# Kernel tuning notes

Measured on AMD Instinct MI355X. Metric: run time of the kernel, lower is better.

The kernel has to match this reference:

```python
import jax, jax.numpy as jnp
import numpy as np

N_NODES = 100000
N_EDGES = 1600000
NODE_F = 128
EDGE_F = 64
OUT = 32
NEG_SLOPE = 0.01  # torch nn.LeakyReLU default


def setup_inputs() -> dict:
    key = jax.random.key(0)
    ks = jax.random.split(key, 7)
    h = jax.random.normal(ks[0], (N_NODES, NODE_F), dtype=jnp.float32)
    edge_feat = jax.random.normal(ks[1], (N_EDGES, EDGE_F), dtype=jnp.float32)
    src = jax.random.randint(ks[2], (N_EDGES,), 0, N_NODES)
    dst = jax.random.randint(ks[3], (N_EDGES,), 0, N_NODES)
    W_node = jax.random.normal(ks[4], (NODE_F, OUT), dtype=jnp.float32) * 0.05
    W_edge = jax.random.normal(ks[5], (EDGE_F, OUT), dtype=jnp.float32) * 0.05
    attn_w = jax.random.normal(ks[6], (3 * OUT,), dtype=jnp.float32) * 0.05
    return {"h": h, "edge_feat": edge_feat, "src": src, "dst": dst,
            "W_node": W_node, "W_edge": W_edge, "attn_w": attn_w}


def reference(h, edge_feat, src, dst, W_node, W_edge, attn_w):
    # Project node and edge features (bias-free linears).
    z = h @ W_node                      # [N, OUT]
    ez = edge_feat @ W_edge             # [E, OUT]

    # attn_fc on cat(src_z, dst_z, edge_z): split weight vector to avoid
    # materializing the [E, 3*OUT] concat.
    a_src, a_dst, a_edge = attn_w[:OUT], attn_w[OUT:2 * OUT], attn_w[2 * OUT:]
    zs = z[src]                         # [E, OUT] gather
    logits = jax.nn.leaky_relu(
        zs @ a_src + z[dst] @ a_dst + ez @ a_edge, NEG_SLOPE)  # [E]

    # Per-destination (segment) softmax over incoming edges.
    seg_max = jax.ops.segment_max(logits, dst, num_segments=N_NODES)
    seg_max = jnp.where(jnp.isfinite(seg_max), seg_max, 0.0)  # empty segments
    e = jnp.exp(logits - seg_max[dst])                          # [E]
    denom = jax.ops.segment_sum(e, dst, num_segments=N_NODES)  # [N]

    # Weighted sum of src z vectors per destination.
    num = jax.ops.segment_sum(e[:, None] * zs, dst, num_segments=N_NODES)
    u = num / jnp.maximum(denom, 1e-20)[:, None]                # [N, OUT]
    return u
```

## Files before the change

kernel.cpp:

```cpp
#include <hip/hip_runtime.h>
#include <hip/hip_bf16.h>

#define N_NODES 100000
#define N_EDGES 1600000
#define NODE_F 128
#define EDGE_F 64
#define OUT_F 32
#define NEG_SLOPE 0.01f
#define NB_SCAN 391

__device__ __forceinline__ unsigned short f2bf(float f) {
    unsigned u = __float_as_uint(f);
    unsigned r = u + 0x7fffu + ((u >> 16) & 1u);
    return (unsigned short)(r >> 16);
}
__device__ __forceinline__ float bf2f(unsigned short b) {
    return __uint_as_float((unsigned)b << 16);
}

__global__ void k_node_proj(const float* __restrict__ h,
                            const float* __restrict__ W_node,
                            const float* __restrict__ attn_w,
                            unsigned short* __restrict__ zb,
                            float* __restrict__ s_src,
                            float* __restrict__ s_dst,
                            int* __restrict__ deg,
                            unsigned long long* __restrict__ scan_state) {
    int gid = blockIdx.x * 256 + threadIdx.x;
    if (gid < N_NODES) deg[gid] = 0;
    if (gid <= NB_SCAN) scan_state[gid] = 0ull;

    __shared__ float Ws[NODE_F * OUT_F];
    for (int i = threadIdx.x; i < NODE_F * OUT_F; i += 256)
        Ws[i] = W_node[i];
    __syncthreads();

    int node = blockIdx.x * 8 + (threadIdx.x >> 5);
    int o = threadIdx.x & 31;
    if (node >= N_NODES) return;

    const float* hrow = h + (size_t)node * NODE_F;
    float acc = 0.f;
#pragma unroll 8
    for (int j = 0; j < NODE_F; ++j)
        acc += hrow[j] * Ws[j * OUT_F + o];

    zb[(size_t)node * OUT_F + o] = f2bf(acc);

    float ps = acc * attn_w[o];
    float pd = acc * attn_w[OUT_F + o];
#pragma unroll
    for (int m = 16; m >= 1; m >>= 1) {
        ps += __shfl_xor(ps, m);
        pd += __shfl_xor(pd, m);
    }
    if (o == 0) {
        s_src[node] = ps;
        s_dst[node] = pd;
    }
}

__global__ void k_edge_dot(const float* __restrict__ edge_feat,
                           const int* __restrict__ dst,
                           const float* __restrict__ W_edge,
                           const float* __restrict__ attn_w,
                           float* __restrict__ g,
                           int* __restrict__ deg) {
    __shared__ float we_s[EDGE_F];
    if (threadIdx.x < EDGE_F) {
        float a = 0.f;
#pragma unroll
        for (int kk = 0; kk < OUT_F; ++kk)
            a += W_edge[threadIdx.x * OUT_F + kk] * attn_w[2 * OUT_F + kk];
        we_s[threadIdx.x] = a;
    }
    __syncthreads();

    int t = blockIdx.x * 256 + threadIdx.x;
    int e = t >> 2;
    int sub = t & 3;
    if (e >= N_EDGES) return;

    const float4* row = (const float4*)(edge_feat + (size_t)e * EDGE_F);
    float acc = 0.f;
#pragma unroll
    for (int i = 0; i < 4; ++i) {
        int fi = sub + i * 4;
        float4 v = row[fi];
        int b = fi * 4;
        acc += v.x * we_s[b] + v.y * we_s[b + 1] + v.z * we_s[b + 2] + v.w * we_s[b + 3];
    }
    acc += __shfl_xor(acc, 1);
    acc += __shfl_xor(acc, 2);

    if (sub == 0) {
        g[e] = acc;
        atomicAdd(deg + dst[e], 1);
    }
}

__global__ __launch_bounds__(256) void k_scan_lookback(
    const int* __restrict__ deg,
    int* __restrict__ offs,
    int* __restrict__ cursor,
    unsigned long long* __restrict__ scan_state) {
    __shared__ int wsum[4];
    __shared__ int bid_s;
    __shared__ int exc_s;

    if (threadIdx.x == 0)
        bid_s = atomicAdd((unsigned int*)&scan_state[NB_SCAN], 1u);
    __syncthreads();
    int bid = bid_s;

    int i = bid * 256 + threadIdx.x;
    int lane = threadIdx.x & 63;
    int wid = threadIdx.x >> 6;
    int v = (i < N_NODES) ? deg[i] : 0;
    int x = v;
#pragma unroll
    for (int d = 1; d < 64; d <<= 1) {
        int y = __shfl_up(x, d);
        if (lane >= d) x += y;
    }
    if (lane == 63) wsum[wid] = x;
    __syncthreads();
    int add = 0;
    for (int w = 0; w < wid; ++w) add += wsum[w];
    int incl = x + add;

    if (threadIdx.x == 0) {
        int bsum = wsum[0] + wsum[1] + wsum[2] + wsum[3];
        if (bid == 0) {
            __hip_atomic_store(&scan_state[0], (2ull << 32) | (unsigned)bsum,
                               __ATOMIC_RELAXED, __HIP_MEMORY_SCOPE_AGENT);
            exc_s = 0;
        } else {
            __hip_atomic_store(&scan_state[bid], (1ull << 32) | (unsigned)bsum,
                               __ATOMIC_RELAXED, __HIP_MEMORY_SCOPE_AGENT);
            int pre = 0;
            for (int j = bid - 1; j >= 0; --j) {
                unsigned long long s;
                do {
                    s = __hip_atomic_load(&scan_state[j], __ATOMIC_RELAXED,
                                          __HIP_MEMORY_SCOPE_AGENT);
                } while ((s >> 32) == 0ull);
                pre += (int)(unsigned)s;
                if ((s >> 32) == 2ull) break;
            }
            __hip_atomic_store(&scan_state[bid],
                               (2ull << 32) | (unsigned)(pre + bsum),
                               __ATOMIC_RELAXED, __HIP_MEMORY_SCOPE_AGENT);
            exc_s = pre;
        }
    }
    __syncthreads();

    if (i < N_NODES) {
        int o = exc_s + incl - v;
        offs[i] = o;
        cursor[i] = o;
    }
}

__global__ void k_scatter(const int* __restrict__ src,
                          const int* __restrict__ dst,
                          const float* __restrict__ g,
                          const float* __restrict__ s_src,
                          const float* __restrict__ s_dst,
                          int* __restrict__ cursor,
                          int2* __restrict__ perm) {
    int e = blockIdx.x * 256 + threadIdx.x;
    if (e >= N_EDGES) return;
    int s = src[e], d = dst[e];
    float logit = s_src[s] + s_dst[d] + g[e];
    logit = logit > 0.f ? logit : NEG_SLOPE * logit;
    float ev = __expf(logit);
    int pos = atomicAdd(cursor + d, 1);
    perm[pos] = make_int2(s, __float_as_int(ev));
}

__global__ void k_node_aggr(const int* __restrict__ offs,
                            const int* __restrict__ cursor,
                            const int2* __restrict__ perm,
                            const unsigned short* __restrict__ zb,
                            float* __restrict__ out) {
    int node = blockIdx.x * 8 + (threadIdx.x >> 5);
    int k = threadIdx.x & 31;
    if (node >= N_NODES) return;

    int start = offs[node];
    int end = cursor[node];

    float acc = 0.f, den_local = 0.f;
    for (int base = start; base < end; base += 32) {
        int idx = base + k;
        int cnt = min(32, end - base);
        float ev = 0.f;
        int sp = 0;
        if (idx < end) {
            int2 pr = perm[idx];
            sp = pr.x;
            ev = __int_as_float(pr.y);
        }
        den_local += ev;
        int j = 0;
        for (; j + 4 <= cnt; j += 4) {
            float e0 = __shfl(ev, j, 32), e1 = __shfl(ev, j + 1, 32);
            float e2 = __shfl(ev, j + 2, 32), e3 = __shfl(ev, j + 3, 32);
            int s0 = __shfl(sp, j, 32), s1 = __shfl(sp, j + 1, 32);
            int s2 = __shfl(sp, j + 2, 32), s3 = __shfl(sp, j + 3, 32);
            float z0 = bf2f(zb[(size_t)s0 * OUT_F + k]);
            float z1 = bf2f(zb[(size_t)s1 * OUT_F + k]);
            float z2 = bf2f(zb[(size_t)s2 * OUT_F + k]);
            float z3 = bf2f(zb[(size_t)s3 * OUT_F + k]);
            acc += e0 * z0;
            acc += e1 * z1;
            acc += e2 * z2;
            acc += e3 * z3;
        }
        for (; j < cnt; ++j) {
            float evj = __shfl(ev, j, 32);
            int sj = __shfl(sp, j, 32);
            acc += evj * bf2f(zb[(size_t)sj * OUT_F + k]);
        }
    }

    float den = den_local;
#pragma unroll
    for (int msk = 16; msk >= 1; msk >>= 1)
        den += __shfl_xor(den, msk, 32);

    out[(size_t)node * OUT_F + k] =
        (end > start) ? acc / fmaxf(den, 1e-20f) : 0.f;
}

extern "C" void kernel_launch(void* const* d_in, const int* in_sizes, int n_in,
                              void* d_out, int out_size, void* d_ws, size_t ws_size,
                              hipStream_t stream) {
    const float* h         = (const float*)d_in[0];
    const float* edge_feat = (const float*)d_in[1];
    const int*   src       = (const int*)d_in[2];
    const int*   dst       = (const int*)d_in[3];
    const float* W_node    = (const float*)d_in[4];
    const float* W_edge    = (const float*)d_in[5];
    const float* attn_w    = (const float*)d_in[6];
    float* out = (float*)d_out;

    char* ws = (char*)d_ws;
    size_t off = 0;
    auto alloc = [&](size_t bytes) {
        void* p = ws + off;
        off += (bytes + 255) & ~(size_t)255;
        return p;
    };
    unsigned short* zb = (unsigned short*)alloc((size_t)N_NODES * OUT_F * sizeof(unsigned short));
    float* s_src  = (float*)alloc((size_t)N_NODES * sizeof(float));
    float* s_dst  = (float*)alloc((size_t)N_NODES * sizeof(float));
    float* g      = (float*)alloc((size_t)N_EDGES * sizeof(float));
    int*   deg    = (int*)alloc((size_t)N_NODES * sizeof(int));
    int*   offs   = (int*)alloc((size_t)N_NODES * sizeof(int));
    int*   cursor = (int*)alloc((size_t)N_NODES * sizeof(int));
    unsigned long long* scan_state =
        (unsigned long long*)alloc((NB_SCAN + 1) * sizeof(unsigned long long));
    int2*  perm   = (int2*)alloc((size_t)N_EDGES * sizeof(int2));

    k_node_proj<<<(N_NODES + 7) / 8, 256, 0, stream>>>(
        h, W_node, attn_w, zb, s_src, s_dst, deg, scan_state);

    {
        int total = N_EDGES * 4;
        k_edge_dot<<<(total + 255) / 256, 256, 0, stream>>>(edge_feat, dst, W_edge, attn_w, g, deg);
    }

    k_scan_lookback<<<NB_SCAN, 256, 0, stream>>>(deg, offs, cursor, scan_state);

    k_scatter<<<(N_EDGES + 255) / 256, 256, 0, stream>>>(
        src, dst, g, s_src, s_dst, cursor, perm);

    k_node_aggr<<<(N_NODES + 7) / 8, 256, 0, stream>>>(
        offs, cursor, perm, zb, out);
}
```

Before: 295.4 us.

## Fuse all pipeline stages into one cooperative persistent kernel with grid syncs

Replaces the five separate launches with a single cooperative kernel of 1024 persistent blocks that runs node projection, edge dot, degree count, block scan, scatter and aggregation, separated by grid-wide barriers. Node and edge projection work is interleaved in one virtual-block loop, and the decoupled lookback scan becomes a two-level scan with a barrier in between. This removes launch gaps and lookback spinning but adds six grid barriers and limits occupancy to a fixed grid. It falls back to the old multi-kernel path if the cooperative launch fails.

```diff
diff --git a/kernel.cpp b/kernel.cpp
--- a/kernel.cpp
+++ b/kernel.cpp
@@ -1,5 +1,8 @@
 #include <hip/hip_runtime.h>
 #include <hip/hip_bf16.h>
+#include <hip/hip_cooperative_groups.h>
+
+namespace cg = cooperative_groups;
 
 #define N_NODES 100000
 #define N_EDGES 1600000
@@ -8,6 +11,7 @@
 #define OUT_F 32
 #define NEG_SLOPE 0.01f
 #define NB_SCAN 391
+#define GRID 1024
 
 __device__ __forceinline__ unsigned short f2bf(float f) {
     unsigned u = __float_as_uint(f);
@@ -16,6 +20,203 @@
 }
 __device__ __forceinline__ float bf2f(unsigned short b) {
     return __uint_as_float((unsigned)b << 16);
+}
+
+__global__ __launch_bounds__(256, 4) void k_mega(
+    const float* __restrict__ h,
+    const float* __restrict__ edge_feat,
+    const int* __restrict__ src,
+    const int* __restrict__ dst,
+    const float* __restrict__ W_node,
+    const float* __restrict__ W_edge,
+    const float* __restrict__ attn_w,
+    unsigned short* __restrict__ zb,
+    float* __restrict__ s_src,
+    float* __restrict__ s_dst,
+    float* __restrict__ g,
+    int* __restrict__ deg,
+    int* __restrict__ offs,
+    int* __restrict__ cursor,
+    int* __restrict__ csum,
+    int* __restrict__ cpre,
+    int2* __restrict__ perm,
+    float* __restrict__ out) {
+    cg::grid_group grid = cg::this_grid();
+    const int tid = threadIdx.x;
+    const int bid = blockIdx.x;
+
+    __shared__ float Ws[NODE_F * OUT_F];
+    __shared__ float we_s[EDGE_F];
+    __shared__ int wsum[4];
+
+    for (int i = tid; i < NODE_F * OUT_F; i += 256) Ws[i] = W_node[i];
+    if (tid < EDGE_F) {
+        float a = 0.f;
+#pragma unroll
+        for (int kk = 0; kk < OUT_F; ++kk)
+            a += W_edge[tid * OUT_F + kk] * attn_w[2 * OUT_F + kk];
+        we_s[tid] = a;
+    }
+    __syncthreads();
+
+    for (int i = bid * 256 + tid; i < N_NODES; i += GRID * 256) deg[i] = 0;
+    grid.sync();
+
+    for (int vb = bid; vb < 37500; vb += GRID) {
+        int p = vb / 3, r = vb - 3 * p;
+        if (r == 0) {
+            int node = p * 8 + (tid >> 5);
+            int o = tid & 31;
+            const float* hrow = h + (size_t)node * NODE_F;
+            float acc = 0.f;
+#pragma unroll 8
+            for (int j = 0; j < NODE_F; ++j)
+                acc += hrow[j] * Ws[j * OUT_F + o];
+            zb[(size_t)node * OUT_F + o] = f2bf(acc);
+            float ps = acc * attn_w[o];
+            float pd = acc * attn_w[OUT_F + o];
+#pragma unroll
+            for (int m = 16; m >= 1; m >>= 1) {
+                ps += __shfl_xor(ps, m, 32);
+                pd += __shfl_xor(pd, m, 32);
+            }
+            if (o == 0) {
+                s_src[node] = ps;
+                s_dst[node] = pd;
+            }
+        } else {
+            int q = 2 * p + (r - 1);
+            int e = q * 64 + (tid >> 2);
+            int sub = tid & 3;
+            const float4* row = (const float4*)(edge_feat + (size_t)e * EDGE_F);
+            float acc = 0.f;
+#pragma unroll
+            for (int i = 0; i < 4; ++i) {
+                int fi = sub + i * 4;
+                float4 v = row[fi];
+                int b = fi * 4;
+                acc += v.x * we_s[b] + v.y * we_s[b + 1] + v.z * we_s[b + 2] + v.w * we_s[b + 3];
+            }
+            acc += __shfl_xor(acc, 1);
+            acc += __shfl_xor(acc, 2);
+            if (sub == 0) {
+                g[e] = acc;
+                atomicAdd(deg + dst[e], 1);
+            }
+        }
+    }
+    grid.sync();
+
+    for (int c = bid; c < NB_SCAN; c += GRID) {
+        int i = c * 256 + tid;
+        int v = (i < N_NODES) ? deg[i] : 0;
+        int lane = tid & 63, wid = tid >> 6;
+        int x = v;
+#pragma unroll
+        for (int d = 1; d < 64; d <<= 1) {
+            int y = __shfl_up(x, d);
+            if (lane >= d) x += y;
+        }
+        if (lane == 63) wsum[wid] = x;
+        __syncthreads();
+        int add = 0;
+        for (int w = 0; w < wid; ++w) add += wsum[w];
+        int incl = x + add;
+        if (i < N_NODES) offs[i] = incl - v;
+        if (tid == 255) csum[c] = incl;
+        __syncthreads();
+    }
+    grid.sync();
+
+    if (bid == 0 && tid < 64) {
+        int base = tid * 7;
+        int loc[7];
+        int lsum = 0;
+#pragma unroll
+        for (int j = 0; j < 7; ++j) {
+            int idx = base + j;
+            int v = (idx < NB_SCAN) ? csum[idx] : 0;
+            loc[j] = lsum;
+            lsum += v;
+        }
+        int x = lsum;
+#pragma unroll
+        for (int d = 1; d < 64; d <<= 1) {
+            int y = __shfl_up(x, d);
+            if (tid >= d) x += y;
+        }
+        int excl = x - lsum;
+#pragma unroll
+        for (int j = 0; j < 7; ++j) {
+            int idx = base + j;
+            if (idx < NB_SCAN) cpre[idx] = excl + loc[j];
+        }
+    }
+    grid.sync();
+
+    for (int i = bid * 256 + tid; i < N_NODES; i += GRID * 256) {
+        int o = offs[i] + cpre[i >> 8];
+        offs[i] = o;
+        cursor[i] = o;
+    }
+    grid.sync();
+
+    for (int e = bid * 256 + tid; e < N_EDGES; e += GRID * 256) {
+        int s = src[e], d = dst[e];
+        float logit = s_src[s] + s_dst[d] + g[e];
+        logit = logit > 0.f ? logit : NEG_SLOPE * logit;
+        float ev = __expf(logit);
+        int pos = atomicAdd(cursor + d, 1);
+        perm[pos] = make_int2(s, __float_as_int(ev));
+    }
+    grid.sync();
+
+    for (int vb = bid; vb < 12500; vb += GRID) {
+        int node = vb * 8 + (tid >> 5);
+        int k = tid & 31;
+        int start = offs[node];
+        int end = cursor[node];
+
+        float acc = 0.f, den_local = 0.f;
+        for (int base = start; base < end; base += 32) {
+            int idx = base + k;
+            int cnt = min(32, end - base);
+            float ev = 0.f;
+            int sp = 0;
+            if (idx < end) {
+                int2 pr = perm[idx];
+                sp = pr.x;
+                ev = __int_as_float(pr.y);
+            }
+            den_local += ev;
+            int j = 0;
+            for (; j + 4 <= cnt; j += 4) {
+                float e0 = __shfl(ev, j, 32), e1 = __shfl(ev, j + 1, 32);
+                float e2 = __shfl(ev, j + 2, 32), e3 = __shfl(ev, j + 3, 32);
+                int s0 = __shfl(sp, j, 32), s1 = __shfl(sp, j + 1, 32);
+                int s2 = __shfl(sp, j + 2, 32), s3 = __shfl(sp, j + 3, 32);
+                float z0 = bf2f(zb[(size_t)s0 * OUT_F + k]);
+                float z1 = bf2f(zb[(size_t)s1 * OUT_F + k]);
+                float z2 = bf2f(zb[(size_t)s2 * OUT_F + k]);
+                float z3 = bf2f(zb[(size_t)s3 * OUT_F + k]);
+                acc += e0 * z0;
+                acc += e1 * z1;
+                acc += e2 * z2;
+                acc += e3 * z3;
+            }
+            for (; j < cnt; ++j) {
+                float evj = __shfl(ev, j, 32);
+                int sj = __shfl(sp, j, 32);
+                acc += evj * bf2f(zb[(size_t)sj * OUT_F + k]);
+            }
+        }
+        float den = den_local;
+#pragma unroll
+        for (int msk = 16; msk >= 1; msk >>= 1)
+            den += __shfl_xor(den, msk, 32);
+        out[(size_t)node * OUT_F + k] =
+            (end > start) ? acc / fmaxf(den, 1e-20f) : 0.f;
+    }
 }
 
 __global__ void k_node_proj(const float* __restrict__ h,
@@ -44,15 +245,13 @@
 #pragma unroll 8
     for (int j = 0; j < NODE_F; ++j)
         acc += hrow[j] * Ws[j * OUT_F + o];
-
     zb[(size_t)node * OUT_F + o] = f2bf(acc);
-
     float ps = acc * attn_w[o];
     float pd = acc * attn_w[OUT_F + o];
 #pragma unroll
     for (int m = 16; m >= 1; m >>= 1) {
-        ps += __shfl_xor(ps, m);
-        pd += __shfl_xor(pd, m);
+        ps += __shfl_xor(ps, m, 32);
+        pd += __shfl_xor(pd, m, 32);
     }
     if (o == 0) {
         s_src[node] = ps;
@@ -75,12 +274,10 @@
         we_s[threadIdx.x] = a;
     }
     __syncthreads();
-
     int t = blockIdx.x * 256 + threadIdx.x;
     int e = t >> 2;
     int sub = t & 3;
     if (e >= N_EDGES) return;
-
     const float4* row = (const float4*)(edge_feat + (size_t)e * EDGE_F);
     float acc = 0.f;
 #pragma unroll
@@ -92,7 +289,6 @@
     }
     acc += __shfl_xor(acc, 1);
     acc += __shfl_xor(acc, 2);
-
     if (sub == 0) {
         g[e] = acc;
         atomicAdd(deg + dst[e], 1);
@@ -107,12 +303,10 @@
     __shared__ int wsum[4];
     __shared__ int bid_s;
     __shared__ int exc_s;
-
     if (threadIdx.x == 0)
         bid_s = atomicAdd((unsigned int*)&scan_state[NB_SCAN], 1u);
     __syncthreads();
     int bid = bid_s;
-
     int i = bid * 256 + threadIdx.x;
     int lane = threadIdx.x & 63;
     int wid = threadIdx.x >> 6;
@@ -128,7 +322,6 @@
     int add = 0;
     for (int w = 0; w < wid; ++w) add += wsum[w];
     int incl = x + add;
-
     if (threadIdx.x == 0) {
         int bsum = wsum[0] + wsum[1] + wsum[2] + wsum[3];
         if (bid == 0) {
@@ -155,7 +348,6 @@
         }
     }
     __syncthreads();
-
     if (i < N_NODES) {
         int o = exc_s + incl - v;
         offs[i] = o;
@@ -188,10 +380,8 @@
     int node = blockIdx.x * 8 + (threadIdx.x >> 5);
     int k = threadIdx.x & 31;
     if (node >= N_NODES) return;
-
     int start = offs[node];
     int end = cursor[node];
-
     float acc = 0.f, den_local = 0.f;
     for (int base = start; base < end; base += 32) {
         int idx = base + k;
@@ -225,12 +415,10 @@
             acc += evj * bf2f(zb[(size_t)sj * OUT_F + k]);
         }
     }
-
     float den = den_local;
 #pragma unroll
     for (int msk = 16; msk >= 1; msk >>= 1)
         den += __shfl_xor(den, msk, 32);
-
     out[(size_t)node * OUT_F + k] =
         (end > start) ? acc / fmaxf(den, 1e-20f) : 0.f;
 }
@@ -261,23 +449,33 @@
     int*   deg    = (int*)alloc((size_t)N_NODES * sizeof(int));
     int*   offs   = (int*)alloc((size_t)N_NODES * sizeof(int));
     int*   cursor = (int*)alloc((size_t)N_NODES * sizeof(int));
+    int*   csum   = (int*)alloc(NB_SCAN * sizeof(int));
+    int*   cpre   = (int*)alloc(NB_SCAN * sizeof(int));
     unsigned long long* scan_state =
         (unsigned long long*)alloc((NB_SCAN + 1) * sizeof(unsigned long long));
     int2*  perm   = (int2*)alloc((size_t)N_EDGES * sizeof(int2));
 
+    void* args[] = {
+        (void*)&h, (void*)&edge_feat, (void*)&src, (void*)&dst,
+        (void*)&W_node, (void*)&W_edge, (void*)&attn_w,
+        (void*)&zb, (void*)&s_src, (void*)&s_dst, (void*)&g,
+        (void*)&deg, (void*)&offs, (void*)&cursor, (void*)&csum, (void*)&cpre,
+        (void*)&perm, (void*)&out
+    };
+    hipError_t err = hipLaunchCooperativeKernel((const void*)k_mega,
+                                                dim3(GRID), dim3(256),
+                                                args, 0, stream);
+    if (err == hipSuccess) return;
+
     k_node_proj<<<(N_NODES + 7) / 8, 256, 0, stream>>>(
         h, W_node, attn_w, zb, s_src, s_dst, deg, scan_state);
-
     {
         int total = N_EDGES * 4;
         k_edge_dot<<<(total + 255) / 256, 256, 0, stream>>>(edge_feat, dst, W_edge, attn_w, g, deg);
     }
-
     k_scan_lookback<<<NB_SCAN, 256, 0, stream>>>(deg, offs, cursor, scan_state);
-
     k_scatter<<<(N_EDGES + 255) / 256, 256, 0, stream>>>(
         src, dst, g, s_src, s_dst, cursor, perm);
-
     k_node_aggr<<<(N_NODES + 7) / 8, 256, 0, stream>>>(
         offs, cursor, perm, zb, out);
 }
```

Result: slower. 911.7 us (+208.6%).

## Fuse logit/exp into edge kernel and scatter only edge indices

Applied to the files above, without the earlier changes.

Computes the leaky-relu logit and exponential inside the edge projection kernel and stores per-edge weights in original edge order. The scatter step now writes only the edge index into the CSR slot instead of a (src, weight) pair. The aggregation kernel gathers src and weight indirectly through that index. This shrinks scatter work and writes but adds two random indirect reads per edge in aggregation.

```diff
diff --git a/kernel.cpp b/kernel.cpp
--- a/kernel.cpp
+++ b/kernel.cpp
@@ -51,8 +51,8 @@
     float pd = acc * attn_w[OUT_F + o];
 #pragma unroll
     for (int m = 16; m >= 1; m >>= 1) {
-        ps += __shfl_xor(ps, m);
-        pd += __shfl_xor(pd, m);
+        ps += __shfl_xor(ps, m, 32);
+        pd += __shfl_xor(pd, m, 32);
     }
     if (o == 0) {
         s_src[node] = ps;
@@ -60,12 +60,15 @@
     }
 }
 
-__global__ void k_edge_dot(const float* __restrict__ edge_feat,
-                           const int* __restrict__ dst,
-                           const float* __restrict__ W_edge,
-                           const float* __restrict__ attn_w,
-                           float* __restrict__ g,
-                           int* __restrict__ deg) {
+__global__ void k_edge_ev(const float* __restrict__ edge_feat,
+                          const int* __restrict__ src,
+                          const int* __restrict__ dst,
+                          const float* __restrict__ W_edge,
+                          const float* __restrict__ attn_w,
+                          const float* __restrict__ s_src,
+                          const float* __restrict__ s_dst,
+                          float* __restrict__ ev_arr,
+                          int* __restrict__ deg) {
     __shared__ float we_s[EDGE_F];
     if (threadIdx.x < EDGE_F) {
         float a = 0.f;
@@ -94,8 +97,11 @@
     acc += __shfl_xor(acc, 2);
 
     if (sub == 0) {
-        g[e] = acc;
-        atomicAdd(deg + dst[e], 1);
+        int s = src[e], d = dst[e];
+        float logit = s_src[s] + s_dst[d] + acc;
+        logit = logit > 0.f ? logit : NEG_SLOPE * logit;
+        ev_arr[e] = __expf(logit);
+        atomicAdd(deg + d, 1);
     }
 }
 
@@ -163,26 +169,20 @@
     }
 }
 
-__global__ void k_scatter(const int* __restrict__ src,
-                          const int* __restrict__ dst,
-                          const float* __restrict__ g,
-                          const float* __restrict__ s_src,
-                          const float* __restrict__ s_dst,
-                          int* __restrict__ cursor,
-                          int2* __restrict__ perm) {
+__global__ void k_scatter_idx(const int* __restrict__ dst,
+                              int* __restrict__ cursor,
+                              int* __restrict__ eidx) {
     int e = blockIdx.x * 256 + threadIdx.x;
     if (e >= N_EDGES) return;
-    int s = src[e], d = dst[e];
-    float logit = s_src[s] + s_dst[d] + g[e];
-    logit = logit > 0.f ? logit : NEG_SLOPE * logit;
-    float ev = __expf(logit);
-    int pos = atomicAdd(cursor + d, 1);
-    perm[pos] = make_int2(s, __float_as_int(ev));
+    int pos = atomicAdd(cursor + dst[e], 1);
+    eidx[pos] = e;
 }
 
 __global__ void k_node_aggr(const int* __restrict__ offs,
                             const int* __restrict__ cursor,
-                            const int2* __restrict__ perm,
+                            const int* __restrict__ eidx,
+                            const int* __restrict__ src,
+                            const float* __restrict__ ev_arr,
                             const unsigned short* __restrict__ zb,
                             float* __restrict__ out) {
     int node = blockIdx.x * 8 + (threadIdx.x >> 5);
@@ -199,9 +199,9 @@
         float ev = 0.f;
         int sp = 0;
         if (idx < end) {
-            int2 pr = perm[idx];
-            sp = pr.x;
-            ev = __int_as_float(pr.y);
+            int ei = eidx[idx];
+            sp = src[ei];
+            ev = ev_arr[ei];
         }
         den_local += ev;
         int j = 0;
@@ -257,27 +257,27 @@
     unsigned short* zb = (unsigned short*)alloc((size_t)N_NODES * OUT_F * sizeof(unsigned short));
     float* s_src  = (float*)alloc((size_t)N_NODES * sizeof(float));
     float* s_dst  = (float*)alloc((size_t)N_NODES * sizeof(float));
-    float* g      = (float*)alloc((size_t)N_EDGES * sizeof(float));
+    float* ev_arr = (float*)alloc((size_t)N_EDGES * sizeof(float));
     int*   deg    = (int*)alloc((size_t)N_NODES * sizeof(int));
     int*   offs   = (int*)alloc((size_t)N_NODES * sizeof(int));
     int*   cursor = (int*)alloc((size_t)N_NODES * sizeof(int));
     unsigned long long* scan_state =
         (unsigned long long*)alloc((NB_SCAN + 1) * sizeof(unsigned long long));
-    int2*  perm   = (int2*)alloc((size_t)N_EDGES * sizeof(int2));
+    int*   eidx   = (int*)alloc((size_t)N_EDGES * sizeof(int));
 
     k_node_proj<<<(N_NODES + 7) / 8, 256, 0, stream>>>(
         h, W_node, attn_w, zb, s_src, s_dst, deg, scan_state);
 
     {
         int total = N_EDGES * 4;
-        k_edge_dot<<<(total + 255) / 256, 256, 0, stream>>>(edge_feat, dst, W_edge, attn_w, g, deg);
+        k_edge_ev<<<(total + 255) / 256, 256, 0, stream>>>(
+            edge_feat, src, dst, W_edge, attn_w, s_src, s_dst, ev_arr, deg);
     }
 
     k_scan_lookback<<<NB_SCAN, 256, 0, stream>>>(deg, offs, cursor, scan_state);
 
-    k_scatter<<<(N_EDGES + 255) / 256, 256, 0, stream>>>(
-        src, dst, g, s_src, s_dst, cursor, perm);
+    k_scatter_idx<<<(N_EDGES + 255) / 256, 256, 0, stream>>>(dst, cursor, eidx);
 
     k_node_aggr<<<(N_NODES + 7) / 8, 256, 0, stream>>>(
-        offs, cursor, perm, zb, out);
-}
+        offs, cursor, eidx, src, ev_arr, zb, out);
+}
```

Measured after the change: 407.4 us. 37.9% more time.
